# Performance work log

Hardware: AMD Instinct MI355X
Metric: run time of the kernel (lower is better)

The kernel has to match this reference:

```python
import jax, jax.numpy as jnp
import numpy as np
from jax import lax

B_, L_, D_MODEL = 2, 2048, 1024
H, P, N, G, K, CHUNK = 32, 64, 128, 1, 4, 256
INTER = H * P                 # 2048
CONV_DIM = INTER + 2 * G * N  # 2304
PROJ = INTER + CONV_DIM + H   # 4384: [gate | hidden_B_C | dt]
EPS = 1e-6


def segment_sum(x):
    # x: [..., T] -> [..., T, T]; segsum[i,j] = sum_{k=j+1..i} x[k] for i>=j, else -inf
    T = x.shape[-1]
    xx = jnp.repeat(x[..., None], T, axis=-1)
    xx = jnp.where(jnp.tril(jnp.ones((T, T), bool), -1), xx, 0.0)
    s = jnp.cumsum(xx, axis=-2)
    return jnp.where(jnp.tril(jnp.ones((T, T), bool)), s, -jnp.inf)


def setup_inputs() -> dict:
    key = jax.random.key(0)
    ks = jax.random.split(key, 6)
    s = 0.02
    return {
        "x": jax.random.normal(ks[0], (B_, L_, D_MODEL), jnp.float32),
        "in_proj_w": jax.random.normal(ks[1], (PROJ, D_MODEL), jnp.float32) * s,
        "conv_w": jax.random.normal(ks[2], (CONV_DIM, 1, K), jnp.float32) * s,
        "conv_b": jnp.zeros((CONV_DIM,), jnp.float32),
        "dt_bias": jax.random.uniform(ks[3], (H,), jnp.float32, 0.0, 1.0),
        "A_log": jnp.log(jnp.arange(1, H + 1, dtype=jnp.float32)),
        "D": jnp.ones((H,), jnp.float32),
        "norm_w": jnp.ones((INTER,), jnp.float32),
        "out_proj_w": jax.random.normal(ks[4], (D_MODEL, INTER), jnp.float32) * s,
    }


def _forward(x, in_proj_w, conv_w, conv_b, dt_bias, A_log, D, norm_w, out_proj_w):
    b, L, _ = x.shape
    proj = x @ in_proj_w.T                                    # [b,L,PROJ]
    gate, hBC, dt = jnp.split(proj, [INTER, INTER + CONV_DIM], axis=-1)
    # depthwise causal conv1d over sequence
    xc = jnp.pad(hBC.transpose(0, 2, 1), ((0, 0), (0, 0), (K - 1, 0)))
    conv = lax.conv_general_dilated(xc, conv_w, (1,), 'VALID',
                                    dimension_numbers=('NCH', 'OIH', 'NCH'),
                                    feature_group_count=CONV_DIM)
    hBC = jax.nn.silu((conv + conv_b[None, :, None]).transpose(0, 2, 1))  # [b,L,CONV_DIM]
    hs, Bm, Cm = jnp.split(hBC, [INTER, INTER + G * N], axis=-1)
    hs = hs.reshape(b, L, H, P)
    Bm = jnp.repeat(Bm.reshape(b, L, G, N), H // G, axis=2)   # [b,L,H,N]
    Cm = jnp.repeat(Cm.reshape(b, L, G, N), H // G, axis=2)
    dt = jax.nn.softplus(dt + dt_bias)                        # [b,L,H]
    A = -jnp.exp(A_log)                                       # [H]
    D_res = hs * D[None, None, :, None]
    hs = hs * dt[..., None]
    Adt = dt * A                                              # [b,L,H]
    c = L // CHUNK
    A_c = Adt.reshape(b, c, CHUNK, H).transpose(0, 3, 1, 2)   # [b,H,c,l]
    A_cum = jnp.cumsum(A_c, axis=-1)
    Lmat = jnp.exp(segment_sum(A_c))                          # [b,H,c,l,l]
    hs_c = hs.reshape(b, c, CHUNK, H, P)
    B_c = Bm.reshape(b, c, CHUNK, H, N)
    C_c = Cm.reshape(b, c, CHUNK, H, N)
    # intra-chunk (diagonal blocks)
    Gm = jnp.einsum('bcshn,bczhn->bchsz', C_c, B_c)
    M = Gm * Lmat.transpose(0, 2, 1, 3, 4)
    Y_diag = jnp.einsum('bchsz,bczhp->bcshp', M, hs_c)
    # per-chunk final states
    decay_states = jnp.exp(A_cum[..., -1:] - A_cum)           # [b,H,c,l]
    B_decay = B_c * decay_states.transpose(0, 2, 3, 1)[..., None]
    states = jnp.einsum('bclhn,bclhp->bchpn', B_decay, hs_c)  # [b,c,H,P,N]
    # inter-chunk recurrence
    decay_chunk = jnp.exp(segment_sum(jnp.pad(A_cum[..., -1], ((0, 0), (0, 0), (1, 0)))))  # [b,H,c+1,c+1]
    states0 = jnp.concatenate([jnp.zeros_like(states[:, :1]), states], axis=1)             # [b,c+1,H,P,N]
    prev = jnp.einsum('bhij,bjhpn->bihpn', decay_chunk, states0)[:, :-1]                   # [b,c,H,P,N]
    # off-diagonal contribution
    state_decay = jnp.exp(A_cum).transpose(0, 2, 3, 1)        # [b,c,l,H]
    Y_off = jnp.einsum('bclhn,bchpn->bclhp', C_c, prev) * state_decay[..., None]
    y = ((Y_diag + Y_off).reshape(b, L, H, P) + D_res).reshape(b, L, INTER)
    # gated grouped RMSNorm (group_size = INTER // G)
    gs = INTER // G
    yf = y.astype(jnp.float32) * jax.nn.silu(gate.astype(jnp.float32))
    yg = yf.reshape(b, L, INTER // gs, gs)
    var = jnp.mean(yg * yg, axis=-1, keepdims=True)
    yn = (yg * lax.rsqrt(var + EPS)).reshape(b, L, INTER) * norm_w
    return yn @ out_proj_w.T


def reference(x, in_proj_w, conv_w, conv_b, dt_bias, A_log, D, norm_w, out_proj_w):
    return _forward(x, in_proj_w, conv_w, conv_b, dt_bias, A_log, D, norm_w, out_proj_w)
```

## Files before the change

### kernel.cpp

```cpp
#include <hip/hip_runtime.h>
#include <stdint.h>

typedef __attribute__((ext_vector_type(8))) short short8;
typedef __attribute__((ext_vector_type(4))) float f32x4;

#define DEV static __device__ __forceinline__

DEV float b2f(unsigned short u) { union { float f; unsigned int i; } x; x.i = ((unsigned int)u) << 16; return x.f; }
DEV unsigned short f2b(float f) {
    union { float f; unsigned int i; } x; x.f = f;
    unsigned int r = x.i + 0x7fffu + ((x.i >> 16) & 1u);
    return (unsigned short)(r >> 16);
}
DEV void gld_lds16(const void* g, void* l) {
    __builtin_amdgcn_global_load_lds((const __attribute__((address_space(1))) void*)g,
                                     (__attribute__((address_space(3))) void*)l, 16, 0, 0);
}
DEV int xcd_swizzle(int bid, int nwg) {
    int q = nwg >> 3, r = nwg & 7;
    int xcd = bid & 7, base = bid >> 3;
    return (xcd < r ? xcd * (q + 1) : r * (q + 1) + (xcd - r) * q) + base;
}

__global__ void cast3_kernel(const float* __restrict__ a, unsigned short* __restrict__ oa, long na8,
                             const float* __restrict__ b, unsigned short* __restrict__ ob_, long nb8,
                             const float* __restrict__ c, unsigned short* __restrict__ oc, long nc8) {
    long i = (long)blockIdx.x * blockDim.x + threadIdx.x;
    long stride = (long)gridDim.x * blockDim.x;
    long tot = na8 + nb8 + nc8;
    for (; i < tot; i += stride) {
        const float* src; unsigned short* dst; long j = i;
        if (j < na8) { src = a; dst = oa; }
        else if (j < na8 + nb8) { j -= na8; src = b; dst = ob_; }
        else { j -= na8 + nb8; src = c; dst = oc; }
        const f32x4* p = (const f32x4*)(src + j * 8);
        f32x4 v0 = p[0], v1 = p[1];
        short8 o;
        o[0] = (short)f2b(v0[0]); o[1] = (short)f2b(v0[1]); o[2] = (short)f2b(v0[2]); o[3] = (short)f2b(v0[3]);
        o[4] = (short)f2b(v1[0]); o[5] = (short)f2b(v1[1]); o[6] = (short)f2b(v1[2]); o[7] = (short)f2b(v1[3]);
        *(short8*)(dst + j * 8) = o;
    }
}

template<int OMODE>
__global__ __launch_bounds__(256) void gemm_nt(
    const unsigned short* __restrict__ A, int lda, long sAy, long sAz,
    const unsigned short* __restrict__ B, int ldb, long sBy, long sBz,
    void* __restrict__ Cp, int ldc, long sCy, long sCz,
    float* __restrict__ aux,
    int M, int N, int K, int tn)
{
    A += (long)blockIdx.y * sAy + (long)blockIdx.z * sAz;
    B += (long)blockIdx.y * sBy + (long)blockIdx.z * sBz;
    int bid = xcd_swizzle(blockIdx.x, gridDim.x);
    int im = bid / tn, in_ = bid % tn;
    int m0 = im * 128, n0 = in_ * 128;
    __shared__ short smem[2 * 2 * 128 * 64];
    int tid = threadIdx.x;
    int lane = tid & 63, wave = tid >> 6;
    int wu = __builtin_amdgcn_readfirstlane(wave);
    int wm = wave >> 1, wn = wave & 1;
    f32x4 acc[4][4];
#pragma unroll
    for (int m = 0; m < 4; m++)
#pragma unroll
        for (int n = 0; n < 4; n++) acc[m][n] = (f32x4){0.f, 0.f, 0.f, 0.f};

    auto stage = [&](int k0, int s) {
        short* As = smem + s * 16384;
        short* Bs = As + 8192;
#pragma unroll
        for (int i = 0; i < 4; ++i) {
            int g = i * 256 + tid;
            int r = g >> 3, pc = g & 7;
            int cc = pc ^ (r & 7);
            gld_lds16(A + (long)(m0 + r) * lda + k0 + cc * 8, As + (i * 256 + wu * 64) * 8);
            int rb = n0 + r; rb = rb < N ? rb : N - 1;
            gld_lds16(B + (long)rb * ldb + k0 + cc * 8, Bs + (i * 256 + wu * 64) * 8);
        }
    };

    int nt = K >> 6;
    stage(0, 0);
    for (int t = 0; t < nt; ++t) {
        int cur = t & 1;
        if (t + 1 < nt) {
            stage((t + 1) << 6, cur ^ 1);
            asm volatile("s_waitcnt vmcnt(8)" ::: "memory");
        } else {
            asm volatile("s_waitcnt vmcnt(0)" ::: "memory");
        }
        __builtin_amdgcn_s_barrier();
        const short* As = smem + cur * 16384;
        const short* Bs = As + 8192;
#pragma unroll
        for (int ks = 0; ks < 2; ++ks) {
            short8 af[4], bfr[4];
#pragma unroll
            for (int m = 0; m < 4; ++m) {
                int r = wm * 64 + m * 16 + (lane & 15);
                int pc = (ks * 4 + (lane >> 4)) ^ (r & 7);
                af[m] = *(const short8*)(As + r * 64 + pc * 8);
            }
#pragma unroll
            for (int n = 0; n < 4; ++n) {
                int r = wn * 64 + n * 16 + (lane & 15);
                int pc = (ks * 4 + (lane >> 4)) ^ (r & 7);
                bfr[n] = *(const short8*)(Bs + r * 64 + pc * 8);
            }
            __builtin_amdgcn_s_setprio(1);
#pragma unroll
            for (int m = 0; m < 4; ++m)
#pragma unroll
                for (int n = 0; n < 4; ++n)
                    acc[m][n] = __builtin_amdgcn_mfma_f32_16x16x32_bf16(af[m], bfr[n], acc[m][n], 0, 0, 0);
            __builtin_amdgcn_s_setprio(0);
        }
        __builtin_amdgcn_s_barrier();
    }

    int rbase = m0 + wm * 64 + ((lane >> 4) << 2);
    int cbase = n0 + wn * 64 + (lane & 15);
    if (OMODE == 0) {
        float* C = (float*)Cp;
        C += (long)blockIdx.y * sCy + (long)blockIdx.z * sCz;
#pragma unroll
        for (int m = 0; m < 4; ++m)
#pragma unroll
            for (int n = 0; n < 4; ++n) {
                int col = cbase + n * 16;
                if (col < N) {
#pragma unroll
                    for (int r = 0; r < 4; ++r)
                        C[(long)(rbase + m * 16 + r) * ldc + col] = acc[m][n][r];
                }
            }
    } else if (OMODE == 4) {
        float* C = (float*)Cp;
#pragma unroll
        for (int m = 0; m < 4; ++m)
#pragma unroll
            for (int r = 0; r < 4; ++r) {
                int row = rbase + m * 16 + r;
                float sc = rsqrtf(aux[row] * (1.f / 2048.f) + 1e-6f);
#pragma unroll
                for (int n = 0; n < 4; ++n)
                    C[(long)row * ldc + cbase + n * 16] = acc[m][n][r] * sc;
            }
    } else if (OMODE == 1) {
        unsigned short* Cs = (unsigned short*)smem;
        int rl = wm * 64 + ((lane >> 4) << 2);
        int cl = wn * 64 + (lane & 15);
#pragma unroll
        for (int m = 0; m < 4; ++m)
#pragma unroll
            for (int r = 0; r < 4; ++r) {
                int row = rl + m * 16 + r;
                int xr = ((row >> 2) & 3) << 4;
#pragma unroll
                for (int n = 0; n < 4; ++n)
                    Cs[row * 128 + ((cl + n * 16) ^ xr)] = f2b(acc[m][n][r]);
            }
        __syncthreads();
        unsigned short* C = (unsigned short*)Cp;
        C += (long)blockIdx.y * sCy + (long)blockIdx.z * sCz;
#pragma unroll
        for (int j = 0; j < 8; ++j) {
            int chunk = j * 256 + tid;
            int row = chunk >> 4, c8 = (chunk & 15) * 8;
            int col = n0 + c8;
            int xr = ((row >> 2) & 3) << 4;
            if (col < N)
                *(short8*)(C + (long)(m0 + row) * ldc + col) = *(const short8*)(Cs + row * 128 + (c8 ^ xr));
        }
    } else {
        if (OMODE == 3) {
#pragma unroll
            for (int m = 0; m < 4; ++m)
#pragma unroll
                for (int n = 0; n < 4; ++n) {
                    int col = cbase + n * 16;
                    if (col >= 4352 && col < N) {
#pragma unroll
                        for (int r = 0; r < 4; ++r)
                            aux[(long)(rbase + m * 16 + r) * 32 + (col - 4352)] = acc[m][n][r];
                    }
                }
        }
        unsigned short* T = (unsigned short*)smem;
        int rl = wm * 64 + ((lane >> 4) << 2);
        int cl = wn * 64 + (lane & 15);
#pragma unroll
        for (int n = 0; n < 4; ++n) {
            int ch = cl + n * 16;
            int sw = (ch & 15) << 3;
#pragma unroll
            for (int m = 0; m < 4; ++m)
#pragma unroll
                for (int r = 0; r < 4; ++r) {
                    int mrow = rl + m * 16 + r;
                    T[ch * 128 + (mrow ^ sw)] = f2b(acc[m][n][r]);
                }
        }
        __syncthreads();
        unsigned short* C = (unsigned short*)Cp;
#pragma unroll
        for (int j = 0; j < 8; ++j) {
            int idx = j * 256 + tid;
            int ch = idx >> 4, mc8 = (idx & 15) * 8;
            int gch = n0 + ch;
            if (gch < N) {
                short8 o = *(const short8*)(T + ch * 128 + (mc8 ^ ((ch & 15) << 3)));
                *(short8*)(C + (long)gch * ldc + m0 + mc8) = o;
            }
        }
    }
}

__global__ __launch_bounds__(256) void dtcum_kernel(
    const float* __restrict__ dtraw,
    const float* __restrict__ dt_bias, const float* __restrict__ A_log,
    float* __restrict__ dtv, float* __restrict__ Acum, float* __restrict__ Atot)
{
    int bh = blockIdx.x;
    int b = bh >> 5, h = bh & 31;
    int tid = threadIdx.x;
    float bias = dt_bias[h];
    float negA = -__expf(A_log[h]);
    __shared__ float s[256];
    for (int c = 0; c < 8; ++c) {
        int t = c * 256 + tid;
        float v = dtraw[(long)(b * 2048 + t) * 32 + h] + bias;
        float dt = v > 20.f ? v : log1pf(__expf(v));
        dtv[(long)bh * 2048 + t] = dt;
        s[tid] = dt * negA;
        __syncthreads();
        for (int off = 1; off < 256; off <<= 1) {
            float x = (tid >= off) ? s[tid - off] : 0.f;
            __syncthreads();
            s[tid] += x;
            __syncthreads();
        }
        Acum[(long)bh * 2048 + t] = s[tid];
        if (tid == 255) Atot[bh * 8 + c] = s[255];
        __syncthreads();
    }
}

__global__ __launch_bounds__(256) void convT_kernel(
    const unsigned short* __restrict__ projT,
    const float* __restrict__ conv_w, const float* __restrict__ conv_b,
    const float* __restrict__ dtv, const float* __restrict__ Acum, const float* __restrict__ Atot,
    unsigned short* __restrict__ xdtT, unsigned short* __restrict__ xdtd,
    unsigned short* __restrict__ Bb, unsigned short* __restrict__ Cb, unsigned short* __restrict__ BT)
{
    int tt = blockIdx.x;
    int cht = blockIdx.y;
    int b = blockIdx.z;
    int t0 = tt * 256;
    int ch0 = cht * 64;
    int tid = threadIdx.x;
    __shared__ short raw[64 * 264];
    __shared__ unsigned short trsp[256 * 64];
    __shared__ float sdt[256], sac[256];
    __shared__ float satot;
    bool hidden = cht < 32;
    for (int j = 0; j < 9; ++j) {
        int idx = j * 256 + tid;
        if (idx < 64 * 33) {
            int r = idx / 33, cc = idx % 33;
            int tg = t0 - 8 + cc * 8;
            short8 v = {0, 0, 0, 0, 0, 0, 0, 0};
            if (tg >= 0)
                v = *(const short8*)(projT + (long)(2048 + ch0 + r) * 4096 + b * 2048 + tg);
            *(short8*)(raw + r * 264 + cc * 8) = v;
        }
    }
    if (hidden) {
        int h = cht;
        sdt[tid] = dtv[(long)(b * 32 + h) * 2048 + t0 + tid];
        sac[tid] = Acum[(long)(b * 32 + h) * 2048 + t0 + tid];
        if (tid == 0) satot = Atot[(b * 32 + h) * 8 + tt];
    }
    __syncthreads();
    for (int p = 0; p < 8; ++p) {
        int ch = p * 8 + (tid >> 5);
        int tb = (tid & 31) * 8;
        int cg = ch0 + ch;
        f32x4 wv = *(const f32x4*)(conv_w + cg * 4);
        float cb = conv_b[cg];
        float s[8];
#pragma unroll
        for (int j = 0; j < 8; ++j) {
            int tl = tb + j;
            float a = cb;
#pragma unroll
            for (int k = 0; k < 4; ++k)
                a += b2f((unsigned short)raw[ch * 264 + tl + 5 + k]) * wv[k];
            s[j] = a / (1.f + __expf(-a));
        }
        if (hidden) {
            short8 o1, o2;
#pragma unroll
            for (int j = 0; j < 8; ++j) {
                int tl = tb + j;
                float xdt = s[j] * sdt[tl];
                float dec = __expf(satot - sac[tl]);
                o1[j] = (short)f2b(xdt);
                o2[j] = (short)f2b(xdt * dec);
            }
            long off = (long)cg * 4096 + b * 2048 + t0 + tb;
            *(short8*)(xdtT + off) = o1;
            *(short8*)(xdtd + off) = o2;
        } else {
            short8 o;
#pragma unroll
            for (int j = 0; j < 8; ++j) o[j] = (short)f2b(s[j]);
            if (cht < 34) {
                int n = (cht - 32) * 64 + ch;
                *(short8*)(BT + (long)n * 4096 + b * 2048 + t0 + tb) = o;
            }
#pragma unroll
            for (int j = 0; j < 8; ++j) {
                int tl = tb + j;
                trsp[tl * 64 + (ch ^ ((tl & 7) << 3))] = (unsigned short)o[j];
            }
        }
    }
    if (!hidden) {
        __syncthreads();
        unsigned short* dst = (cht < 34) ? Bb : Cb;
        int n0 = ((cht - 32) & 1) * 64;
        for (int p = 0; p < 8; ++p) {
            int idx = p * 256 + tid;
            int tl = idx >> 3, c8 = (idx & 7) * 8;
            short8 o;
#pragma unroll
            for (int q = 0; q < 8; ++q)
                o[q] = (short)trsp[tl * 64 + ((c8 + q) ^ ((tl & 7) << 3))];
            *(short8*)(dst + (long)(b * 2048 + t0 + tl) * 128 + n0 + c8) = o;
        }
    }
}

__global__ __launch_bounds__(256) void ydiagoff_kernel(
    const unsigned short* __restrict__ Gm,
    const float* __restrict__ Acum,
    const unsigned short* __restrict__ xdtT,
    const unsigned short* __restrict__ projT,
    const unsigned short* __restrict__ Cb,
    const unsigned short* __restrict__ prevb,
    const float* __restrict__ dtv,
    const float* __restrict__ Dp,
    const float* __restrict__ norm_w,
    unsigned short* __restrict__ ynu,
    float* __restrict__ ssq)
{
    int blk = blockIdx.x;
    int h = blk & 31, bc = blk >> 5;
    int c = bc & 7, b = bc >> 3;
    int tid = threadIdx.x, lane = tid & 63, wave = tid >> 6;
    __shared__ float sAc[256];
    __shared__ short Mb[256 * 64];
    __shared__ float sdi[256];
    float Dv = Dp[h];
    sAc[tid] = Acum[(long)(b * 32 + h) * 2048 + c * 256 + tid];
    sdi[tid] = Dv / dtv[(long)(b * 32 + h) * 2048 + c * 256 + tid];
    __syncthreads();
    f32x4 acc[4][4];
#pragma unroll
    for (int m = 0; m < 4; m++)
#pragma unroll
        for (int n = 0; n < 4; n++) acc[m][n] = (f32x4){0.f, 0.f, 0.f, 0.f};

    for (int zp = 0; zp < 4; ++zp) {
#pragma unroll
        for (int i = 0; i < 8; ++i) {
            int ci = i * 256 + tid;
            int s = ci >> 3, cz = ci & 7;
            int z0 = zp * 64 + cz * 8;
            short8 gv = *(const short8*)(Gm + ((long)bc * 256 + s) * 256 + z0);
            float as = sAc[s];
            short8 o;
#pragma unroll
            for (int j = 0; j < 8; ++j) {
                int z = z0 + j;
                float e = (s >= z) ? __expf(as - sAc[z]) : 0.f;
                float mval = b2f((unsigned short)gv[j]) * e;
                if (s == z) mval += sdi[s];
                o[j] = (short)f2b(mval);
            }
            *(short8*)(Mb + s * 64 + (cz ^ (s & 7)) * 8) = o;
        }
        __syncthreads();
#pragma unroll
        for (int ks = 0; ks < 2; ++ks) {
            short8 af[4], bfr[4];
#pragma unroll
            for (int m = 0; m < 4; ++m) {
                int r = wave * 64 + m * 16 + (lane & 15);
                int pc = (ks * 4 + (lane >> 4)) ^ (r & 7);
                af[m] = *(const short8*)(Mb + r * 64 + pc * 8);
            }
#pragma unroll
            for (int n = 0; n < 4; ++n) {
                int p = n * 16 + (lane & 15);
                int zcol = c * 256 + zp * 64 + ks * 32 + (lane >> 4) * 8;
                bfr[n] = *(const short8*)(xdtT + (long)(h * 64 + p) * 4096 + b * 2048 + zcol);
            }
#pragma unroll
            for (int m = 0; m < 4; ++m)
#pragma unroll
                for (int n = 0; n < 4; ++n)
                    acc[m][n] = __builtin_amdgcn_mfma_f32_16x16x32_bf16(af[m], bfr[n], acc[m][n], 0, 0, 0);
        }
        __syncthreads();
    }
    float el[4];
#pragma unroll
    for (int m = 0; m < 4; ++m) el[m] = __expf(sAc[wave * 64 + m * 16 + (lane & 15)]);
#pragma unroll
    for (int ks = 0; ks < 4; ++ks) {
        short8 af[4], bfr[4];
#pragma unroll
        for (int m = 0; m < 4; ++m) {
            int l = wave * 64 + m * 16 + (lane & 15);
            short8 cv = *(const short8*)(Cb + ((long)b * 2048 + c * 256 + l) * 128 + ks * 32 + (lane >> 4) * 8);
#pragma unroll
            for (int j = 0; j < 8; ++j) af[m][j] = (short)f2b(b2f((unsigned short)cv[j]) * el[m]);
        }
#pragma unroll
        for (int n = 0; n < 4; ++n) {
            int p = n * 16 + (lane & 15);
            bfr[n] = *(const short8*)(prevb + ((long)(bc * 32 + h) * 64 + p) * 128 + ks * 32 + (lane >> 4) * 8);
        }
#pragma unroll
        for (int m = 0; m < 4; ++m)
#pragma unroll
            for (int n = 0; n < 4; ++n)
                acc[m][n] = __builtin_amdgcn_mfma_f32_16x16x32_bf16(af[m], bfr[n], acc[m][n], 0, 0, 0);
    }
    unsigned short* gt = (unsigned short*)Mb;
#pragma unroll
    for (int i = 0; i < 8; ++i) {
        int idx = i * 256 + tid;
        int r = idx >> 5, c8 = (idx & 31) * 8;
        short8 v = *(const short8*)(projT + (long)(h * 64 + r) * 4096 + b * 2048 + c * 256 + c8);
#pragma unroll
        for (int j = 0; j < 8; ++j)
            gt[r * 256 + ((c8 + j) ^ ((r & 7) << 3))] = (unsigned short)v[j];
    }
    __syncthreads();
#pragma unroll
    for (int m = 0; m < 4; ++m)
#pragma unroll
        for (int r = 0; r < 4; ++r) {
            int tl = wave * 64 + m * 16 + ((lane >> 4) << 2) + r;
            long bt = (long)b * 2048 + c * 256 + tl;
            float part = 0.f;
#pragma unroll
            for (int n = 0; n < 4; ++n) {
                int cl = n * 16 + (lane & 15);
                int ch = h * 64 + cl;
                float yv = acc[m][n][r];
                float g = b2f(gt[cl * 256 + (tl ^ ((cl & 7) << 3))]);
                float yf = yv * g / (1.f + __expf(-g));
                part += yf * yf;
                ynu[bt * 2048 + ch] = f2b(yf * norm_w[ch]);
            }
#pragma unroll
            for (int w2 = 1; w2 < 16; w2 <<= 1) part += __shfl_xor(part, w2);
            if ((lane & 15) == 0) atomicAdd(&ssq[bt], part);
        }
}

__global__ __launch_bounds__(256) void scan_kernel(
    const float* __restrict__ states,
    const float* __restrict__ Atot,
    unsigned short* __restrict__ prevb)
{
    int bh = blockIdx.x;
    int b = bh >> 5, h = bh & 31;
    float ex[8];
#pragma unroll
    for (int c = 0; c < 8; ++c) ex[c] = __expf(Atot[bh * 8 + c]);
    for (int e = threadIdx.x; e < 8192; e += 256) {
        float S = 0.f;
#pragma unroll
        for (int c = 0; c < 8; ++c) {
            long idx = (long)((b * 8 + c) * 32 + h) * 8192 + e;
            prevb[idx] = f2b(S);
            S = ex[c] * S + states[idx];
        }
    }
}

extern "C" void kernel_launch(void* const* d_in, const int* in_sizes, int n_in,
                              void* d_out, int out_size, void* d_ws, size_t ws_size,
                              hipStream_t stream)
{
    const float* x        = (const float*)d_in[0];
    const float* in_proj  = (const float*)d_in[1];
    const float* conv_w   = (const float*)d_in[2];
    const float* conv_b   = (const float*)d_in[3];
    const float* dt_bias  = (const float*)d_in[4];
    const float* A_log    = (const float*)d_in[5];
    const float* Dp       = (const float*)d_in[6];
    const float* norm_w   = (const float*)d_in[7];
    const float* out_proj = (const float*)d_in[8];
    float* out = (float*)d_out;

    char* w = (char*)d_ws;
    auto alloc = [&](size_t bytes) { char* p = w; w += (bytes + 255) & ~(size_t)255; return p; };
    unsigned short* xb    = (unsigned short*)alloc(4096L * 1024 * 2);
    unsigned short* wb    = (unsigned short*)alloc(4384L * 1024 * 2);
    unsigned short* ob    = (unsigned short*)alloc(1024L * 2048 * 2);
    unsigned short* projT = (unsigned short*)alloc(4384L * 4096 * 2);
    float*          dtraw = (float*)        alloc(4096L * 32 * 4);
    float*          dtv   = (float*)        alloc(64L * 2048 * 4);
    float*          Acum  = (float*)        alloc(64L * 2048 * 4);
    float*          Atot  = (float*)        alloc(64L * 8 * 4);
    unsigned short* xdtT  = (unsigned short*)alloc(2048L * 4096 * 2);
    unsigned short* xdtd  = (unsigned short*)alloc(2048L * 4096 * 2);
    unsigned short* Bb    = (unsigned short*)alloc(4096L * 128 * 2);
    unsigned short* Cb    = (unsigned short*)alloc(4096L * 128 * 2);
    unsigned short* BT    = (unsigned short*)alloc(128L * 4096 * 2);
    unsigned short* Gmb   = (unsigned short*)alloc(16L * 256 * 256 * 2);
    float*          states= (float*)        alloc(2L * 8 * 2048 * 128 * 4);
    unsigned short* prevb = (unsigned short*)alloc(2L * 8 * 2048 * 128 * 2);
    unsigned short* ynu   = (unsigned short*)alloc(4096L * 2048 * 2);
    float*          ssq   = (float*)        alloc(4096L * 4);

    hipMemsetAsync(ssq, 0, 4096 * 4, stream);

    cast3_kernel<<<2048, 256, 0, stream>>>(x, xb, 4096L * 1024 / 8,
                                           in_proj, wb, 4384L * 1024 / 8,
                                           out_proj, ob, 1024L * 2048 / 8);

    gemm_nt<3><<<dim3(32 * 35, 1, 1), 256, 0, stream>>>(
        xb, 1024, 0, 0, wb, 1024, 0, 0, projT, 4096, 0, 0, dtraw, 4096, 4384, 1024, 35);

    dtcum_kernel<<<64, 256, 0, stream>>>(dtraw, dt_bias, A_log, dtv, Acum, Atot);

    convT_kernel<<<dim3(8, 36, 2), 256, 0, stream>>>(
        projT, conv_w, conv_b, dtv, Acum, Atot, xdtT, xdtd, Bb, Cb, BT);

    gemm_nt<1><<<dim3(4, 8, 2), 256, 0, stream>>>(
        Cb, 128, 256L * 128, 2048L * 128,
        Bb, 128, 256L * 128, 2048L * 128,
        Gmb, 256, 256L * 256, 8L * 256 * 256, nullptr, 256, 256, 128, 2);

    gemm_nt<0><<<dim3(16, 8, 2), 256, 0, stream>>>(
        xdtd, 4096, 256, 2048,
        BT, 4096, 256, 2048,
        states, 128, 2048L * 128, 8L * 2048 * 128, nullptr, 2048, 128, 256, 1);

    scan_kernel<<<64, 256, 0, stream>>>(states, Atot, prevb);

    ydiagoff_kernel<<<512, 256, 0, stream>>>(Gmb, Acum, xdtT, projT, Cb, prevb,
                                             dtv, Dp, norm_w, ynu, ssq);

    gemm_nt<4><<<dim3(32 * 8, 1, 1), 256, 0, stream>>>(
        ynu, 2048, 0, 0, ob, 2048, 0, 0, out, 1024, 0, 0, ssq, 4096, 1024, 2048, 8);
}
```

Measured before the change: 311.9 us.

## Skip upper-triangular blocks in chunk kernel and stage ynu stores through LDS

The intra-chunk kernel now builds the masked decay matrix only for rows at or below each 64-wide z panel, and skips the MFMAs for 16-row tiles that lie entirely above the diagonal. This removes causally masked work. Exponentials switch to exp2f on log2e-prescaled cumulative A values, and norm_w is cached in shared memory. The gated output is staged in a padded LDS tile and written out as coalesced 16-byte rows instead of scattered 2-byte stores, at the cost of extra LDS and a barrier. The OMODE==3 guard around the aux write is also removed.

```diff
diff --git a/kernel.cpp b/kernel.cpp
--- a/kernel.cpp
+++ b/kernel.cpp
@@ -5,6 +5,7 @@
 typedef __attribute__((ext_vector_type(4))) float f32x4;
 
 #define DEV static __device__ __forceinline__
+#define LOG2E 1.44269504088896340736f
 
 DEV float b2f(unsigned short u) { union { float f; unsigned int i; } x; x.i = ((unsigned int)u) << 16; return x.f; }
 DEV unsigned short f2b(float f) {
@@ -174,19 +175,17 @@
                 *(short8*)(C + (long)(m0 + row) * ldc + col) = *(const short8*)(Cs + row * 128 + (c8 ^ xr));
         }
     } else {
-        if (OMODE == 3) {
-#pragma unroll
-            for (int m = 0; m < 4; ++m)
-#pragma unroll
-                for (int n = 0; n < 4; ++n) {
-                    int col = cbase + n * 16;
-                    if (col >= 4352 && col < N) {
-#pragma unroll
-                        for (int r = 0; r < 4; ++r)
-                            aux[(long)(rbase + m * 16 + r) * 32 + (col - 4352)] = acc[m][n][r];
-                    }
+#pragma unroll
+        for (int m = 0; m < 4; ++m)
+#pragma unroll
+            for (int n = 0; n < 4; ++n) {
+                int col = cbase + n * 16;
+                if (col >= 4352 && col < N) {
+#pragma unroll
+                    for (int r = 0; r < 4; ++r)
+                        aux[(long)(rbase + m * 16 + r) * 32 + (col - 4352)] = acc[m][n][r];
                 }
-        }
+            }
         unsigned short* T = (unsigned short*)smem;
         int rl = wm * 64 + ((lane >> 4) << 2);
         int cl = wn * 64 + (lane & 15);
@@ -363,9 +362,12 @@
     __shared__ float sAc[256];
     __shared__ short Mb[256 * 64];
     __shared__ float sdi[256];
+    __shared__ float snw[64];
+    __shared__ unsigned short yt[256 * 72];
     float Dv = Dp[h];
-    sAc[tid] = Acum[(long)(b * 32 + h) * 2048 + c * 256 + tid];
+    sAc[tid] = Acum[(long)(b * 32 + h) * 2048 + c * 256 + tid] * LOG2E;
     sdi[tid] = Dv / dtv[(long)(b * 32 + h) * 2048 + c * 256 + tid];
+    if (tid < 64) snw[tid] = norm_w[h * 64 + tid];
     __syncthreads();
     f32x4 acc[4][4];
 #pragma unroll
@@ -373,19 +375,21 @@
 #pragma unroll
         for (int n = 0; n < 4; n++) acc[m][n] = (f32x4){0.f, 0.f, 0.f, 0.f};
 
+#pragma unroll
     for (int zp = 0; zp < 4; ++zp) {
-#pragma unroll
-        for (int i = 0; i < 8; ++i) {
+        const int z0 = zp * 64;
+        const int niter = 8 - zp * 2;
+        for (int i = 0; i < niter; ++i) {
             int ci = i * 256 + tid;
-            int s = ci >> 3, cz = ci & 7;
-            int z0 = zp * 64 + cz * 8;
-            short8 gv = *(const short8*)(Gm + ((long)bc * 256 + s) * 256 + z0);
+            int s = z0 + (ci >> 3), cz = ci & 7;
+            int zc0 = z0 + cz * 8;
+            short8 gv = *(const short8*)(Gm + ((long)bc * 256 + s) * 256 + zc0);
             float as = sAc[s];
             short8 o;
 #pragma unroll
             for (int j = 0; j < 8; ++j) {
-                int z = z0 + j;
-                float e = (s >= z) ? __expf(as - sAc[z]) : 0.f;
+                int z = zc0 + j;
+                float e = (s >= z) ? exp2f(as - sAc[z]) : 0.f;
                 float mval = b2f((unsigned short)gv[j]) * e;
                 if (s == z) mval += sdi[s];
                 o[j] = (short)f2b(mval);
@@ -398,27 +402,32 @@
             short8 af[4], bfr[4];
 #pragma unroll
             for (int m = 0; m < 4; ++m) {
-                int r = wave * 64 + m * 16 + (lane & 15);
-                int pc = (ks * 4 + (lane >> 4)) ^ (r & 7);
-                af[m] = *(const short8*)(Mb + r * 64 + pc * 8);
+                if (wave * 64 + m * 16 >= z0) {
+                    int r = wave * 64 + m * 16 + (lane & 15);
+                    int pc = (ks * 4 + (lane >> 4)) ^ (r & 7);
+                    af[m] = *(const short8*)(Mb + r * 64 + pc * 8);
+                }
             }
 #pragma unroll
             for (int n = 0; n < 4; ++n) {
                 int p = n * 16 + (lane & 15);
-                int zcol = c * 256 + zp * 64 + ks * 32 + (lane >> 4) * 8;
+                int zcol = c * 256 + z0 + ks * 32 + (lane >> 4) * 8;
                 bfr[n] = *(const short8*)(xdtT + (long)(h * 64 + p) * 4096 + b * 2048 + zcol);
             }
 #pragma unroll
-            for (int m = 0; m < 4; ++m)
-#pragma unroll
-                for (int n = 0; n < 4; ++n)
-                    acc[m][n] = __builtin_amdgcn_mfma_f32_16x16x32_bf16(af[m], bfr[n], acc[m][n], 0, 0, 0);
+            for (int m = 0; m < 4; ++m) {
+                if (wave * 64 + m * 16 >= z0) {
+#pragma unroll
+                    for (int n = 0; n < 4; ++n)
+                        acc[m][n] = __builtin_amdgcn_mfma_f32_16x16x32_bf16(af[m], bfr[n], acc[m][n], 0, 0, 0);
+                }
+            }
         }
         __syncthreads();
     }
     float el[4];
 #pragma unroll
-    for (int m = 0; m < 4; ++m) el[m] = __expf(sAc[wave * 64 + m * 16 + (lane & 15)]);
+    for (int m = 0; m < 4; ++m) el[m] = exp2f(sAc[wave * 64 + m * 16 + (lane & 15)]);
 #pragma unroll
     for (int ks = 0; ks < 4; ++ks) {
         short8 af[4], bfr[4];
@@ -461,17 +470,24 @@
 #pragma unroll
             for (int n = 0; n < 4; ++n) {
                 int cl = n * 16 + (lane & 15);
-                int ch = h * 64 + cl;
                 float yv = acc[m][n][r];
                 float g = b2f(gt[cl * 256 + (tl ^ ((cl & 7) << 3))]);
                 float yf = yv * g / (1.f + __expf(-g));
                 part += yf * yf;
-                ynu[bt * 2048 + ch] = f2b(yf * norm_w[ch]);
+                yt[tl * 72 + cl] = f2b(yf * snw[cl]);
             }
 #pragma unroll
             for (int w2 = 1; w2 < 16; w2 <<= 1) part += __shfl_xor(part, w2);
             if ((lane & 15) == 0) atomicAdd(&ssq[bt], part);
         }
+    __syncthreads();
+#pragma unroll
+    for (int j = 0; j < 8; ++j) {
+        int idx = j * 256 + tid;
+        int tl = idx >> 3, c8 = (idx & 7) * 8;
+        short8 o = *(const short8*)(yt + tl * 72 + c8);
+        *(short8*)(ynu + ((long)b * 2048 + c * 256 + tl) * 2048 + h * 64 + c8) = o;
+    }
 }
 
 __global__ __launch_bounds__(256) void scan_kernel(
```

Measured after the change: 296.3 us. -5.0%, faster.
